# Kernel tuning notes

Hardware: AMD Instinct MI355X
Metric: run time of the kernel (lower is better)

## Reference

```python
import jax, jax.numpy as jnp
import numpy as np

CHUNK = 128


def setup_inputs() -> dict:
    key = jax.random.key(0)
    ks = jax.random.split(key, 10)
    B, L, d, n = 4, 2048, 192, 64
    sd = 1.0 / np.sqrt(d)
    return {
        "x": jax.random.normal(ks[0], (B, L, d), dtype=jnp.float32),
        "A_log": -jnp.log(2.0) + 0.1 * jax.random.normal(ks[1], (d,), dtype=jnp.float32),
        "W_B": sd * jax.random.normal(ks[2], (n, d), dtype=jnp.float32),
        "W_C": sd * jax.random.normal(ks[3], (n, d), dtype=jnp.float32),
        "W_dt": sd * jax.random.normal(ks[4], (d, d), dtype=jnp.float32),
        "b_dt": 0.1 * jax.random.normal(ks[5], (d,), dtype=jnp.float32),
        "W_xp": sd * jax.random.normal(ks[6], (2 * d, d), dtype=jnp.float32),
        "b_xp": 0.1 * jax.random.normal(ks[7], (2 * d,), dtype=jnp.float32),
        "W_out": sd * jax.random.normal(ks[8], (d, d), dtype=jnp.float32),
        "b_out": 0.1 * jax.random.normal(ks[9], (d,), dtype=jnp.float32),
    }


def reference(x, A_log, W_B, W_C, W_dt, b_dt, W_xp, b_xp, W_out, b_out):
    p = CHUNK
    b, l, d = x.shape
    n = W_B.shape[0]
    pad = (-l) % p
    xp = jnp.pad(x, ((0, 0), (0, pad), (0, 0))) if pad > 0 else x
    c = xp.shape[1] // p

    A = -jnp.exp(A_log)                                   # (d,)
    proj = xp @ W_xp.T + b_xp                             # (b, Lp, 2d)
    x_bar, z = jnp.split(proj, 2, axis=-1)
    Bm = x_bar @ W_B.T                                    # (b, Lp, n)
    Cm = x_bar @ W_C.T                                    # (b, Lp, n)
    dt = jax.nn.softplus(x_bar @ W_dt.T + b_dt)           # (b, Lp, d)
    A_bar = jnp.exp(dt * A)                               # (b, Lp, d)

    resh = lambda t: t.reshape(b, c, p, t.shape[-1])
    xc, Bc, Cc, Ac = resh(x_bar), resh(Bm), resh(Cm), resh(A_bar)

    # intra-chunk: masked decay matrix M[b,c,i,j,d]
    log_A = jnp.log(jnp.abs(Ac) + 1e-8)
    la_cum = jnp.cumsum(log_A, axis=2)                    # (b,c,p,d)
    log_M = la_cum[:, :, :, None, :] - la_cum[:, :, None, :, :]
    causal = jnp.tril(jnp.ones((p, p), dtype=x.dtype))
    M = jnp.exp(log_M) * causal[None, None, :, :, None]   # (b,c,p,p,d)
    G = jnp.einsum('bcin,bcjn->bcij', Cc, Bc)             # C_i . B_j
    # same math as einsum('bcpn,bcpnd->bcpd', C, einsum('bcijd,bcjnd->bcind', M, B x))
    y_intra = jnp.einsum('bcij,bcijd,bcjd->bcid', G, M, xc)

    # inter-chunk recurrence over chunk states
    chunk_A = jnp.prod(Ac, axis=2)                        # (b,c,d)
    chunk_states = jnp.einsum('bcpn,bcpd->bcnd', Bc, xc * Ac)

    def step(state, inp):
        ca, cs = inp                                       # (b,d), (b,n,d)
        return state * ca[:, None, :] + cs, state          # emit state BEFORE update

    _, prev = jax.lax.scan(
        step,
        jnp.zeros((b, n, d), dtype=x.dtype),
        (jnp.moveaxis(chunk_A, 1, 0), jnp.moveaxis(chunk_states, 1, 0)),
    )
    prev = jnp.moveaxis(prev, 0, 1)                       # (b,c,n,d)
    y_inter = jnp.einsum('bcpn,bcnd->bcpd', Cc, prev)

    y = (y_intra + y_inter).reshape(b, c * p, d)[:, :l]
    y = y * jax.nn.silu(z[:, :l])
    return y @ W_out.T + b_out
```

## Files before the change

kernel.cpp:

```cpp
#include <hip/hip_runtime.h>
#include <math.h>

#define TOK      8192
#define DIM      192
#define NST      64
#define PCHUNK   128
#define NCHUNKS  64
#define CPB      16
#define BATCH    4
#define SUB      32
#define NSUB     4
#define NG       4
#define NPG      16

typedef __attribute__((ext_vector_type(8))) short  bf16x8;
typedef __attribute__((ext_vector_type(4))) float  f32x4;

__device__ __forceinline__ unsigned short f2bf(float f) {
    unsigned int u = __float_as_uint(f);
    u += 0x7fff + ((u >> 16) & 1);
    return (unsigned short)(u >> 16);
}
__device__ __forceinline__ float bf2f(unsigned short h) {
    return __uint_as_float(((unsigned int)h) << 16);
}

__global__ __launch_bounds__(256)
void cast_kernel(const float* __restrict__ x,   const float* __restrict__ Wxp,
                 const float* __restrict__ WB,  const float* __restrict__ WC,
                 const float* __restrict__ Wdt, const float* __restrict__ Wout,
                 unsigned short* __restrict__ xb,     unsigned short* __restrict__ wxpb,
                 unsigned short* __restrict__ wbcdtb, unsigned short* __restrict__ woutb)
{
    int u = blockIdx.x * 256 + threadIdx.x;
    const float* src; unsigned short* dst; int idx;
    if      (u < 393216) { src = x;    dst = xb;             idx = u; }
    else if (u < 411648) { src = Wxp;  dst = wxpb;           idx = u - 393216; }
    else if (u < 414720) { src = WB;   dst = wbcdtb;         idx = u - 411648; }
    else if (u < 417792) { src = WC;   dst = wbcdtb + 12288; idx = u - 414720; }
    else if (u < 427008) { src = Wdt;  dst = wbcdtb + 24576; idx = u - 417792; }
    else if (u < 436224) { src = Wout; dst = woutb;          idx = u - 427008; }
    else return;
    float4 v = *(const float4*)(src + (size_t)idx * 4);
    ushort4 r; r.x = f2bf(v.x); r.y = f2bf(v.y); r.z = f2bf(v.z); r.w = f2bf(v.w);
    *(ushort4*)(dst + (size_t)idx * 4) = r;
}

__device__ __forceinline__
void mfma_64x64(const unsigned short* __restrict__ X, int ldx,
                const unsigned short* __restrict__ W, int K,
                int m_wave, int n0, int lr, int kg, f32x4 acc[4][4])
{
    for (int k0 = 0; k0 < K; k0 += 32) {
        bf16x8 af[4], bfr[4];
        #pragma unroll
        for (int mi = 0; mi < 4; ++mi)
            af[mi] = *(const bf16x8*)(X + (size_t)(m_wave + mi*16 + lr) * ldx + k0 + kg*8);
        #pragma unroll
        for (int ni = 0; ni < 4; ++ni)
            bfr[ni] = *(const bf16x8*)(W + (size_t)(n0 + ni*16 + lr) * K + k0 + kg*8);
        #pragma unroll
        for (int mi = 0; mi < 4; ++mi)
            #pragma unroll
            for (int ni = 0; ni < 4; ++ni)
                acc[mi][ni] = __builtin_amdgcn_mfma_f32_16x16x32_bf16(
                                  af[mi], bfr[ni], acc[mi][ni], 0, 0, 0);
    }
}

__global__ __launch_bounds__(256)
void proj_gemm(const unsigned short* __restrict__ xb,
               const unsigned short* __restrict__ wxpb,
               const float* __restrict__ b_xp,
               float* __restrict__ proj, unsigned short* __restrict__ projb)
{
    const int lane = threadIdx.x & 63, wave = threadIdx.x >> 6;
    const int m_wave = blockIdx.x * 256 + wave * 64;
    const int n0 = blockIdx.y * 64;
    const int lr = lane & 15, kg = lane >> 4;
    f32x4 acc[4][4] = {};
    mfma_64x64(xb, DIM, wxpb, DIM, m_wave, n0, lr, kg, acc);
    #pragma unroll
    for (int ni = 0; ni < 4; ++ni) {
        int col = n0 + ni*16 + lr;
        float bias = b_xp[col];
        #pragma unroll
        for (int mi = 0; mi < 4; ++mi)
            #pragma unroll
            for (int r = 0; r < 4; ++r) {
                int row = m_wave + mi*16 + kg*4 + r;
                float v = acc[mi][ni][r] + bias;
                proj [(size_t)row * 384 + col] = v;
                projb[(size_t)row * 384 + col] = f2bf(v);
            }
    }
}

__global__ __launch_bounds__(256)
void bcdt_gemm(const unsigned short* __restrict__ projb,
               const unsigned short* __restrict__ wbcdtb,
               const float* __restrict__ b_dt, const float* __restrict__ A_log,
               float* __restrict__ BC, float* __restrict__ Abar)
{
    const int lane = threadIdx.x & 63, wave = threadIdx.x >> 6;
    const int m_wave = blockIdx.x * 256 + wave * 64;
    const int n0 = blockIdx.y * 64;
    const int lr = lane & 15, kg = lane >> 4;
    f32x4 acc[4][4] = {};
    mfma_64x64(projb, 384, wbcdtb, DIM, m_wave, n0, lr, kg, acc);
    if (n0 < 128) {
        #pragma unroll
        for (int ni = 0; ni < 4; ++ni) {
            int col = n0 + ni*16 + lr;
            #pragma unroll
            for (int mi = 0; mi < 4; ++mi)
                #pragma unroll
                for (int r = 0; r < 4; ++r) {
                    int row = m_wave + mi*16 + kg*4 + r;
                    BC[(size_t)row * 128 + col] = acc[mi][ni][r];
                }
        }
    } else {
        #pragma unroll
        for (int ni = 0; ni < 4; ++ni) {
            int c2 = n0 - 128 + ni*16 + lr;
            float bias = b_dt[c2];
            float Av = -expf(A_log[c2]);
            #pragma unroll
            for (int mi = 0; mi < 4; ++mi)
                #pragma unroll
                for (int r = 0; r < 4; ++r) {
                    int row = m_wave + mi*16 + kg*4 + r;
                    float v = acc[mi][ni][r] + bias;
                    float sp = (v > 20.f) ? v : log1pf(expf(v));
                    Abar[(size_t)row * DIM + c2] = expf(sp * Av);
                }
        }
    }
}

__global__ __launch_bounds__(256)
void out_gemm(const unsigned short* __restrict__ ygb,
              const unsigned short* __restrict__ woutb,
              const float* __restrict__ b_out, float* __restrict__ out)
{
    const int lane = threadIdx.x & 63, wave = threadIdx.x >> 6;
    const int m_wave = blockIdx.x * 256 + wave * 64;
    const int n0 = blockIdx.y * 64;
    const int lr = lane & 15, kg = lane >> 4;
    f32x4 acc[4][4] = {};
    mfma_64x64(ygb, DIM, woutb, DIM, m_wave, n0, lr, kg, acc);
    #pragma unroll
    for (int ni = 0; ni < 4; ++ni) {
        int col = n0 + ni*16 + lr;
        float bias = b_out[col];
        #pragma unroll
        for (int mi = 0; mi < 4; ++mi)
            #pragma unroll
            for (int r = 0; r < 4; ++r) {
                int row = m_wave + mi*16 + kg*4 + r;
                out[(size_t)row * DIM + col] = acc[mi][ni][r] + bias;
            }
    }
}

__global__ __launch_bounds__(192)
void state_kernel(const float* __restrict__ proj,
                  const float* __restrict__ Abar,
                  const float* __restrict__ Bm,
                  float* __restrict__ S,
                  float* __restrict__ R,
                  float* __restrict__ dprod)
{
    int bc = blockIdx.x, s = blockIdx.y, g = blockIdx.z;
    int dd = threadIdx.x;
    int t0 = bc * PCHUNK + s * SUB;
    __shared__ float Bs[SUB][NPG];
    if (threadIdx.x < SUB * NPG / 4) {
        int row = threadIdx.x >> 2, c4 = threadIdx.x & 3;
        *(float4*)&Bs[row][c4 * 4] =
            *(const float4*)(Bm + (size_t)(t0 + row) * 128 + g * NPG + c4 * 4);
    }
    __syncthreads();
    float H[NPG] = {}, Rr[NPG] = {};
    float cp = 1.f;
    float a_cur = fabsf(Abar[(size_t)t0 * DIM + dd]) + 1e-8f;
    float x_cur = proj[(size_t)t0 * 384 + dd];
    for (int i = 0; i < SUB; ++i) {
        float a_nxt = 0.f, x_nxt = 0.f;
        if (i + 1 < SUB) {
            a_nxt = fabsf(Abar[(size_t)(t0 + i + 1) * DIM + dd]) + 1e-8f;
            x_nxt = proj[(size_t)(t0 + i + 1) * 384 + dd];
        }
        cp *= a_cur;
        float4 b0 = *(const float4*)&Bs[i][0];
        float4 b1 = *(const float4*)&Bs[i][4];
        float4 b2 = *(const float4*)&Bs[i][8];
        float4 b3 = *(const float4*)&Bs[i][12];
        float bb[NPG] = {b0.x,b0.y,b0.z,b0.w, b1.x,b1.y,b1.z,b1.w,
                         b2.x,b2.y,b2.z,b2.w, b3.x,b3.y,b3.z,b3.w};
        #pragma unroll
        for (int j = 0; j < NPG; ++j) {
            float u = bb[j] * x_cur;
            H[j]  = fmaf(a_cur, H[j], u);
            Rr[j] = fmaf(u, a_cur, Rr[j]);
        }
        a_cur = a_nxt; x_cur = x_nxt;
    }
    size_t base = (((size_t)(bc * NSUB + s)) * NST + g * NPG) * DIM + dd;
    #pragma unroll
    for (int j = 0; j < NPG; ++j) {
        S[base + (size_t)j * DIM] = H[j];
        R[base + (size_t)j * DIM] = Rr[j];
    }
    if (g == 0) dprod[(size_t)(bc * NSUB + s) * DIM + dd] = cp;
}

__global__ __launch_bounds__(256)
void reduce_kernel(const float* __restrict__ dprod,
                   const float* __restrict__ R,
                   float* __restrict__ cA,
                   float* __restrict__ Rsum)
{
    int u = blockIdx.x * 256 + threadIdx.x;
    const int NR = NCHUNKS * NST * 48;
    if (u < NR) {
        int dd = (u % 48) * 4;
        int nn = (u / 48) % NST;
        int bc = u / (48 * NST);
        const size_t Q2 = (size_t)NST * DIM;
        size_t so = ((size_t)(bc * NSUB) * NST + nn) * DIM + dd;
        float4 acc = {0.f, 0.f, 0.f, 0.f};
        #pragma unroll
        for (int s = 0; s < NSUB; ++s) {
            float4 v = *(const float4*)(R + so + (size_t)s * Q2);
            acc.x += v.x; acc.y += v.y; acc.z += v.z; acc.w += v.w;
        }
        *(float4*)(Rsum + ((size_t)bc * NST + nn) * DIM + dd) = acc;
    } else if (u < NR + NCHUNKS * 48) {
        int v = u - NR;
        int dd = (v % 48) * 4;
        int bc = v / 48;
        float4 acc = {1.f, 1.f, 1.f, 1.f};
        #pragma unroll
        for (int s = 0; s < NSUB; ++s) {
            float4 dp = *(const float4*)(dprod + (size_t)(bc * NSUB + s) * DIM + dd);
            acc.x *= dp.x; acc.y *= dp.y; acc.z *= dp.z; acc.w *= dp.w;
        }
        *(float4*)(cA + (size_t)bc * DIM + dd) = acc;
    }
}

__global__ __launch_bounds__(256)
void scan_kernel(const float* __restrict__ cA,
                 const float* __restrict__ Rsum,
                 float* __restrict__ prev)
{
    int v = blockIdx.x * 256 + threadIdx.x;
    if (v >= BATCH * NST * 48) return;
    int dd = (v % 48) * 4;
    int nn = (v / 48) % NST;
    int b  = v / (48 * NST);
    int bc0 = b * CPB;
    float4 st = {0.f, 0.f, 0.f, 0.f};
    float4 a_cur = *(const float4*)(cA + (size_t)bc0 * DIM + dd);
    float4 r_cur = *(const float4*)(Rsum + ((size_t)bc0 * NST + nn) * DIM + dd);
    for (int c = 0; c < CPB; ++c) {
        int bc = bc0 + c;
        float4 a_nxt = {0,0,0,0}, r_nxt = {0,0,0,0};
        if (c + 1 < CPB) {
            a_nxt = *(const float4*)(cA + (size_t)(bc + 1) * DIM + dd);
            r_nxt = *(const float4*)(Rsum + ((size_t)(bc + 1) * NST + nn) * DIM + dd);
        }
        *(float4*)(prev + ((size_t)bc * NST + nn) * DIM + dd) = st;
        st.x = fmaf(st.x, a_cur.x, r_cur.x);
        st.y = fmaf(st.y, a_cur.y, r_cur.y);
        st.z = fmaf(st.z, a_cur.z, r_cur.z);
        st.w = fmaf(st.w, a_cur.w, r_cur.w);
        a_cur = a_nxt; r_cur = r_nxt;
    }
}

__global__ __launch_bounds__(192)
void intra_kernel(const float* __restrict__ proj,
                  const float* __restrict__ Abar,
                  const float* __restrict__ Bm,
                  const float* __restrict__ Cm,
                  const float* __restrict__ prev,
                  const float* __restrict__ S,
                  const float* __restrict__ dprod,
                  unsigned short* __restrict__ p_y)
{
    int bc = blockIdx.x, s = blockIdx.y, g = blockIdx.z;
    int dd = threadIdx.x;
    int t0 = bc * PCHUNK + s * SUB;
    __shared__ float Bs[SUB][NPG];
    __shared__ float Cs[SUB][NPG];
    if (threadIdx.x < SUB * NPG / 2) {
    }
    {
        int nunits = SUB * NPG / 4;
        for (int idx = threadIdx.x; idx < 2 * nunits; idx += 192) {
            int m = idx >= nunits;
            int q = idx - m * nunits;
            int row = q >> 2, c4 = q & 3;
            const float* src = (m ? Cm : Bm) + (size_t)(t0 + row) * 128
                             + (m ? 64 : 0) + g * NPG + c4 * 4;
            float4 v = *(const float4*)src;
            if (m) *(float4*)&Cs[row][c4 * 4] = v;
            else   *(float4*)&Bs[row][c4 * 4] = v;
        }
    }
    float H[NPG] = {}, P[NPG];
    for (int k = 0; k < s; ++k) {
        float dpk = dprod[(size_t)(bc * NSUB + k) * DIM + dd];
        size_t sb = (((size_t)(bc * NSUB + k)) * NST + g * NPG) * DIM + dd;
        #pragma unroll
        for (int j = 0; j < NPG; ++j)
            H[j] = fmaf(H[j], dpk, S[sb + (size_t)j * DIM]);
    }
    #pragma unroll
    for (int j = 0; j < NPG; ++j)
        P[j] = prev[((size_t)bc * NST + g * NPG + j) * DIM + dd];
    __syncthreads();

    float a_cur = fabsf(Abar[(size_t)t0 * DIM + dd]) + 1e-8f;
    float x_cur = proj[(size_t)t0 * 384 + dd];
    for (int i = 0; i < SUB; ++i) {
        int t = t0 + i;
        float a_nxt = 0.f, x_nxt = 0.f;
        if (i + 1 < SUB) {
            a_nxt = fabsf(Abar[(size_t)(t + 1) * DIM + dd]) + 1e-8f;
            x_nxt = proj[(size_t)(t + 1) * 384 + dd];
        }
        float4 b0 = *(const float4*)&Bs[i][0];
        float4 b1 = *(const float4*)&Bs[i][4];
        float4 b2 = *(const float4*)&Bs[i][8];
        float4 b3 = *(const float4*)&Bs[i][12];
        float4 c0 = *(const float4*)&Cs[i][0];
        float4 c1 = *(const float4*)&Cs[i][4];
        float4 c2 = *(const float4*)&Cs[i][8];
        float4 c3 = *(const float4*)&Cs[i][12];
        float bb[NPG] = {b0.x,b0.y,b0.z,b0.w, b1.x,b1.y,b1.z,b1.w,
                         b2.x,b2.y,b2.z,b2.w, b3.x,b3.y,b3.z,b3.w};
        float cc[NPG] = {c0.x,c0.y,c0.z,c0.w, c1.x,c1.y,c1.z,c1.w,
                         c2.x,c2.y,c2.z,c2.w, c3.x,c3.y,c3.z,c3.w};
        float ya[4] = {0.f, 0.f, 0.f, 0.f};
        #pragma unroll
        for (int j = 0; j < NPG; ++j) {
            H[j] = fmaf(a_cur, H[j], bb[j] * x_cur);
            ya[j & 3] = fmaf(cc[j], H[j] + P[j], ya[j & 3]);
        }
        p_y[((size_t)g * TOK + t) * DIM + dd] = f2bf((ya[0] + ya[1]) + (ya[2] + ya[3]));
        a_cur = a_nxt; x_cur = x_nxt;
    }
}

__global__ __launch_bounds__(256)
void gate_kernel(const unsigned short* __restrict__ p_y,
                 const float* __restrict__ proj,
                 unsigned short* __restrict__ ygb)
{
    int v = blockIdx.x * 256 + threadIdx.x;
    if (v >= TOK * 48) return;
    int t = v / 48;
    int dd = (v % 48) * 4;
    const size_t Q = (size_t)TOK * DIM;
    size_t off = (size_t)t * DIM + dd;
    float acc[4] = {0.f, 0.f, 0.f, 0.f};
    #pragma unroll
    for (int gidx = 0; gidx < NG; ++gidx) {
        ushort4 y = *(const ushort4*)(p_y + off + (size_t)gidx * Q);
        acc[0] += bf2f(y.x); acc[1] += bf2f(y.y);
        acc[2] += bf2f(y.z); acc[3] += bf2f(y.w);
    }
    float4 z = *(const float4*)(proj + (size_t)t * 384 + DIM + dd);
    ushort4 r;
    r.x = f2bf(acc[0] * (z.x / (1.f + expf(-z.x))));
    r.y = f2bf(acc[1] * (z.y / (1.f + expf(-z.y))));
    r.z = f2bf(acc[2] * (z.z / (1.f + expf(-z.z))));
    r.w = f2bf(acc[3] * (z.w / (1.f + expf(-z.w))));
    *(ushort4*)(ygb + off) = r;
}

extern "C" void kernel_launch(void* const* d_in, const int* in_sizes, int n_in,
                              void* d_out, int out_size, void* d_ws, size_t ws_size,
                              hipStream_t stream)
{
    (void)in_sizes; (void)n_in; (void)out_size; (void)ws_size;
    const float* x     = (const float*)d_in[0];
    const float* A_log = (const float*)d_in[1];
    const float* W_B   = (const float*)d_in[2];
    const float* W_C   = (const float*)d_in[3];
    const float* W_dt  = (const float*)d_in[4];
    const float* b_dt  = (const float*)d_in[5];
    const float* W_xp  = (const float*)d_in[6];
    const float* b_xp  = (const float*)d_in[7];
    const float* W_out = (const float*)d_in[8];
    const float* b_out = (const float*)d_in[9];
    float* out = (float*)d_out;

    char* w = (char*)d_ws;
    auto take = [&](size_t bytes) { char* p = w; w += (bytes + 255) & ~(size_t)255; return p; };
    float*          proj   = (float*)         take((size_t)TOK*384*4);
    unsigned short* projb  = (unsigned short*)take((size_t)TOK*384*2);
    unsigned short* xb     = (unsigned short*)take((size_t)TOK*DIM*2);
    unsigned short* wxpb   = (unsigned short*)take((size_t)384*DIM*2);
    unsigned short* wbcdtb = (unsigned short*)take((size_t)320*DIM*2);
    unsigned short* woutb  = (unsigned short*)take((size_t)DIM*DIM*2);
    float*          BC     = (float*)         take((size_t)TOK*128*4);
    float*          Abar   = (float*)         take((size_t)TOK*DIM*4);
    float*          dprod  = (float*)         take((size_t)NCHUNKS*NSUB*DIM*4);
    float*          cAc    = (float*)         take((size_t)NCHUNKS*DIM*4);
    float*          prev   = (float*)         take((size_t)NCHUNKS*NST*DIM*4);
    float*          Rsum   = (float*)         take((size_t)NCHUNKS*NST*DIM*4);
    float*          Sarr   = (float*)         take((size_t)NCHUNKS*NSUB*NST*DIM*4);
    float*          Rarr   = (float*)         take((size_t)NCHUNKS*NSUB*NST*DIM*4);
    unsigned short* p_y    = (unsigned short*)take((size_t)NG*TOK*DIM*2);
    unsigned short* ygb    = (unsigned short*)take((size_t)TOK*DIM*2);
    const float* Bm = BC;
    const float* Cm = BC;
    dim3 blk(256);

    cast_kernel<<<dim3((436224 + 255)/256), blk, 0, stream>>>(
        x, W_xp, W_B, W_C, W_dt, W_out, xb, wxpb, wbcdtb, woutb);
    proj_gemm<<<dim3(TOK/256, 384/64), blk, 0, stream>>>(xb, wxpb, b_xp, proj, projb);
    bcdt_gemm<<<dim3(TOK/256, 320/64), blk, 0, stream>>>(projb, wbcdtb, b_dt, A_log, BC, Abar);
    state_kernel<<<dim3(NCHUNKS, NSUB, NG), dim3(192), 0, stream>>>(
        proj, Abar, Bm, Sarr, Rarr, dprod);
    reduce_kernel<<<dim3((NCHUNKS*NST*48 + NCHUNKS*48 + 255)/256), blk, 0, stream>>>(
        dprod, Rarr, cAc, Rsum);
    scan_kernel<<<dim3((BATCH*NST*48 + 255)/256), blk, 0, stream>>>(cAc, Rsum, prev);
    intra_kernel<<<dim3(NCHUNKS, NSUB, NG), dim3(192), 0, stream>>>(
        proj, Abar, Bm, Cm, prev, Sarr, dprod, p_y);
    gate_kernel<<<dim3((TOK*48 + 255)/256), blk, 0, stream>>>(p_y, proj, ygb);
    out_gemm<<<dim3(TOK/256, DIM/64), blk, 0, stream>>>(ygb, woutb, b_out, out);
}
```

Baseline: 179.2 us.

## Fold x_bar projection into B/C/dt weights and halve state groups

Precomputes combined weights W_{B,C,dt}·W_xp[:d] and the matching biases in the prep kernel, so the B/C/dt GEMM reads bf16 x directly instead of waiting on a bf16 copy of proj. The x/z GEMM now writes separate fp32 x_bar and z arrays and drops the bf16 proj output. State groups change from 4×16 to 2×32 states per thread, which halves the partial-y traffic in the gate kernel but raises register pressure in the scan kernels. The fabs on Abar is removed because exp always yields positive values. Bf16 rounding of the combined weights slightly changes numerics.

```diff
diff --git a/kernel.cpp b/kernel.cpp
--- a/kernel.cpp
+++ b/kernel.cpp
@@ -10,8 +10,8 @@
 #define BATCH    4
 #define SUB      32
 #define NSUB     4
-#define NG       4
-#define NPG      16
+#define NG       2
+#define NPG      32
 
 typedef __attribute__((ext_vector_type(8))) short  bf16x8;
 typedef __attribute__((ext_vector_type(4))) float  f32x4;
@@ -25,25 +25,52 @@
     return __uint_as_float(((unsigned int)h) << 16);
 }
 
-__global__ __launch_bounds__(256)
-void cast_kernel(const float* __restrict__ x,   const float* __restrict__ Wxp,
+#define XU      393216
+#define WXPU    18432
+#define WOUTU   9216
+#define CAST_U  (XU + WXPU + WOUTU)
+#define WCOMB_N 61440
+#define PREP_N  (CAST_U + WCOMB_N + 320)
+
+__global__ __launch_bounds__(256)
+void prep_kernel(const float* __restrict__ x,   const float* __restrict__ Wxp,
                  const float* __restrict__ WB,  const float* __restrict__ WC,
                  const float* __restrict__ Wdt, const float* __restrict__ Wout,
+                 const float* __restrict__ b_xp, const float* __restrict__ b_dt,
                  unsigned short* __restrict__ xb,     unsigned short* __restrict__ wxpb,
-                 unsigned short* __restrict__ wbcdtb, unsigned short* __restrict__ woutb)
+                 unsigned short* __restrict__ woutb,  unsigned short* __restrict__ wcombb,
+                 float* __restrict__ biasC)
 {
     int u = blockIdx.x * 256 + threadIdx.x;
-    const float* src; unsigned short* dst; int idx;
-    if      (u < 393216) { src = x;    dst = xb;             idx = u; }
-    else if (u < 411648) { src = Wxp;  dst = wxpb;           idx = u - 393216; }
-    else if (u < 414720) { src = WB;   dst = wbcdtb;         idx = u - 411648; }
-    else if (u < 417792) { src = WC;   dst = wbcdtb + 12288; idx = u - 414720; }
-    else if (u < 427008) { src = Wdt;  dst = wbcdtb + 24576; idx = u - 417792; }
-    else if (u < 436224) { src = Wout; dst = woutb;          idx = u - 427008; }
-    else return;
-    float4 v = *(const float4*)(src + (size_t)idx * 4);
-    ushort4 r; r.x = f2bf(v.x); r.y = f2bf(v.y); r.z = f2bf(v.z); r.w = f2bf(v.w);
-    *(ushort4*)(dst + (size_t)idx * 4) = r;
+    if (u < CAST_U) {
+        const float* src; unsigned short* dst; int idx;
+        if      (u < XU)          { src = x;    dst = xb;    idx = u; }
+        else if (u < XU + WXPU)   { src = Wxp;  dst = wxpb;  idx = u - XU; }
+        else                      { src = Wout; dst = woutb; idx = u - XU - WXPU; }
+        float4 v = *(const float4*)(src + (size_t)idx * 4);
+        ushort4 r; r.x = f2bf(v.x); r.y = f2bf(v.y); r.z = f2bf(v.z); r.w = f2bf(v.w);
+        *(ushort4*)(dst + (size_t)idx * 4) = r;
+    } else if (u < CAST_U + WCOMB_N) {
+        int idx = u - CAST_U;
+        int n = idx / DIM, k = idx % DIM;
+        const float* wr = (n < 64) ? WB + (size_t)n * DIM
+                        : (n < 128) ? WC + (size_t)(n - 64) * DIM
+                                    : Wdt + (size_t)(n - 128) * DIM;
+        float acc = 0.f;
+        for (int j = 0; j < DIM; ++j)
+            acc = fmaf(wr[j], Wxp[(size_t)j * DIM + k], acc);
+        wcombb[(size_t)n * DIM + k] = f2bf(acc);
+    } else if (u < PREP_N) {
+        int n = u - CAST_U - WCOMB_N;
+        const float* wr = (n < 64) ? WB + (size_t)n * DIM
+                        : (n < 128) ? WC + (size_t)(n - 64) * DIM
+                                    : Wdt + (size_t)(n - 128) * DIM;
+        float acc = 0.f;
+        for (int j = 0; j < DIM; ++j)
+            acc = fmaf(wr[j], b_xp[j], acc);
+        if (n >= 128) acc += b_dt[n - 128];
+        biasC[n] = acc;
+    }
 }
 
 __device__ __forceinline__
@@ -69,10 +96,10 @@
 }
 
 __global__ __launch_bounds__(256)
-void proj_gemm(const unsigned short* __restrict__ xb,
-               const unsigned short* __restrict__ wxpb,
-               const float* __restrict__ b_xp,
-               float* __restrict__ proj, unsigned short* __restrict__ projb)
+void xz_gemm(const unsigned short* __restrict__ xb,
+             const unsigned short* __restrict__ wxpb,
+             const float* __restrict__ b_xp,
+             float* __restrict__ xbar, float* __restrict__ zarr)
 {
     const int lane = threadIdx.x & 63, wave = threadIdx.x >> 6;
     const int m_wave = blockIdx.x * 256 + wave * 64;
@@ -80,6 +107,8 @@
     const int lr = lane & 15, kg = lane >> 4;
     f32x4 acc[4][4] = {};
     mfma_64x64(xb, DIM, wxpb, DIM, m_wave, n0, lr, kg, acc);
+    float* dst = (n0 < DIM) ? xbar : zarr;
+    int cofs = (n0 < DIM) ? 0 : DIM;
     #pragma unroll
     for (int ni = 0; ni < 4; ++ni) {
         int col = n0 + ni*16 + lr;
@@ -89,17 +118,15 @@
             #pragma unroll
             for (int r = 0; r < 4; ++r) {
                 int row = m_wave + mi*16 + kg*4 + r;
-                float v = acc[mi][ni][r] + bias;
-                proj [(size_t)row * 384 + col] = v;
-                projb[(size_t)row * 384 + col] = f2bf(v);
+                dst[(size_t)row * DIM + col - cofs] = acc[mi][ni][r] + bias;
             }
     }
 }
 
 __global__ __launch_bounds__(256)
-void bcdt_gemm(const unsigned short* __restrict__ projb,
-               const unsigned short* __restrict__ wbcdtb,
-               const float* __restrict__ b_dt, const float* __restrict__ A_log,
+void bcdt_gemm(const unsigned short* __restrict__ xb,
+               const unsigned short* __restrict__ wcombb,
+               const float* __restrict__ biasC, const float* __restrict__ A_log,
                float* __restrict__ BC, float* __restrict__ Abar)
 {
     const int lane = threadIdx.x & 63, wave = threadIdx.x >> 6;
@@ -107,24 +134,26 @@
     const int n0 = blockIdx.y * 64;
     const int lr = lane & 15, kg = lane >> 4;
     f32x4 acc[4][4] = {};
-    mfma_64x64(projb, 384, wbcdtb, DIM, m_wave, n0, lr, kg, acc);
+    mfma_64x64(xb, DIM, wcombb, DIM, m_wave, n0, lr, kg, acc);
     if (n0 < 128) {
         #pragma unroll
         for (int ni = 0; ni < 4; ++ni) {
             int col = n0 + ni*16 + lr;
+            float bias = biasC[col];
             #pragma unroll
             for (int mi = 0; mi < 4; ++mi)
                 #pragma unroll
                 for (int r = 0; r < 4; ++r) {
                     int row = m_wave + mi*16 + kg*4 + r;
-                    BC[(size_t)row * 128 + col] = acc[mi][ni][r];
+                    BC[(size_t)row * 128 + col] = acc[mi][ni][r] + bias;
                 }
         }
     } else {
         #pragma unroll
         for (int ni = 0; ni < 4; ++ni) {
-            int c2 = n0 - 128 + ni*16 + lr;
-            float bias = b_dt[c2];
+            int col = n0 + ni*16 + lr;
+            int c2 = col - 128;
+            float bias = biasC[col];
             float Av = -expf(A_log[c2]);
             #pragma unroll
             for (int mi = 0; mi < 4; ++mi)
@@ -165,7 +194,7 @@
 }
 
 __global__ __launch_bounds__(192)
-void state_kernel(const float* __restrict__ proj,
+void state_kernel(const float* __restrict__ xbar,
                   const float* __restrict__ Abar,
                   const float* __restrict__ Bm,
                   float* __restrict__ S,
@@ -176,34 +205,31 @@
     int dd = threadIdx.x;
     int t0 = bc * PCHUNK + s * SUB;
     __shared__ float Bs[SUB][NPG];
-    if (threadIdx.x < SUB * NPG / 4) {
-        int row = threadIdx.x >> 2, c4 = threadIdx.x & 3;
+    for (int q = threadIdx.x; q < SUB * NPG / 4; q += 192) {
+        int row = q >> 3, c4 = q & 7;
         *(float4*)&Bs[row][c4 * 4] =
             *(const float4*)(Bm + (size_t)(t0 + row) * 128 + g * NPG + c4 * 4);
     }
     __syncthreads();
     float H[NPG] = {}, Rr[NPG] = {};
     float cp = 1.f;
-    float a_cur = fabsf(Abar[(size_t)t0 * DIM + dd]) + 1e-8f;
-    float x_cur = proj[(size_t)t0 * 384 + dd];
+    float a_cur = Abar[(size_t)t0 * DIM + dd] + 1e-8f;
+    float x_cur = xbar[(size_t)t0 * DIM + dd];
     for (int i = 0; i < SUB; ++i) {
         float a_nxt = 0.f, x_nxt = 0.f;
         if (i + 1 < SUB) {
-            a_nxt = fabsf(Abar[(size_t)(t0 + i + 1) * DIM + dd]) + 1e-8f;
-            x_nxt = proj[(size_t)(t0 + i + 1) * 384 + dd];
+            a_nxt = Abar[(size_t)(t0 + i + 1) * DIM + dd] + 1e-8f;
+            x_nxt = xbar[(size_t)(t0 + i + 1) * DIM + dd];
         }
         cp *= a_cur;
-        float4 b0 = *(const float4*)&Bs[i][0];
-        float4 b1 = *(const float4*)&Bs[i][4];
-        float4 b2 = *(const float4*)&Bs[i][8];
-        float4 b3 = *(const float4*)&Bs[i][12];
-        float bb[NPG] = {b0.x,b0.y,b0.z,b0.w, b1.x,b1.y,b1.z,b1.w,
-                         b2.x,b2.y,b2.z,b2.w, b3.x,b3.y,b3.z,b3.w};
-        #pragma unroll
-        for (int j = 0; j < NPG; ++j) {
-            float u = bb[j] * x_cur;
-            H[j]  = fmaf(a_cur, H[j], u);
-            Rr[j] = fmaf(u, a_cur, Rr[j]);
+        #pragma unroll
+        for (int q = 0; q < NPG / 4; ++q) {
+            float4 b = *(const float4*)&Bs[i][q * 4];
+            float u0 = b.x * x_cur, u1 = b.y * x_cur, u2 = b.z * x_cur, u3 = b.w * x_cur;
+            H[q*4+0] = fmaf(a_cur, H[q*4+0], u0); Rr[q*4+0] = fmaf(u0, a_cur, Rr[q*4+0]);
+            H[q*4+1] = fmaf(a_cur, H[q*4+1], u1); Rr[q*4+1] = fmaf(u1, a_cur, Rr[q*4+1]);
+            H[q*4+2] = fmaf(a_cur, H[q*4+2], u2); Rr[q*4+2] = fmaf(u2, a_cur, Rr[q*4+2]);
+            H[q*4+3] = fmaf(a_cur, H[q*4+3], u3); Rr[q*4+3] = fmaf(u3, a_cur, Rr[q*4+3]);
         }
         a_cur = a_nxt; x_cur = x_nxt;
     }
@@ -282,10 +308,9 @@
 }
 
 __global__ __launch_bounds__(192)
-void intra_kernel(const float* __restrict__ proj,
+void intra_kernel(const float* __restrict__ xbar,
                   const float* __restrict__ Abar,
-                  const float* __restrict__ Bm,
-                  const float* __restrict__ Cm,
+                  const float* __restrict__ BC,
                   const float* __restrict__ prev,
                   const float* __restrict__ S,
                   const float* __restrict__ dprod,
@@ -296,15 +321,13 @@
     int t0 = bc * PCHUNK + s * SUB;
     __shared__ float Bs[SUB][NPG];
     __shared__ float Cs[SUB][NPG];
-    if (threadIdx.x < SUB * NPG / 2) {
-    }
     {
         int nunits = SUB * NPG / 4;
         for (int idx = threadIdx.x; idx < 2 * nunits; idx += 192) {
             int m = idx >= nunits;
             int q = idx - m * nunits;
-            int row = q >> 2, c4 = q & 3;
-            const float* src = (m ? Cm : Bm) + (size_t)(t0 + row) * 128
+            int row = q >> 3, c4 = q & 7;
+            const float* src = BC + (size_t)(t0 + row) * 128
                              + (m ? 64 : 0) + g * NPG + c4 * 4;
             float4 v = *(const float4*)src;
             if (m) *(float4*)&Cs[row][c4 * 4] = v;
@@ -324,32 +347,28 @@
         P[j] = prev[((size_t)bc * NST + g * NPG + j) * DIM + dd];
     __syncthreads();
 
-    float a_cur = fabsf(Abar[(size_t)t0 * DIM + dd]) + 1e-8f;
-    float x_cur = proj[(size_t)t0 * 384 + dd];
+    float a_cur = Abar[(size_t)t0 * DIM + dd] + 1e-8f;
+    float x_cur = xbar[(size_t)t0 * DIM + dd];
     for (int i = 0; i < SUB; ++i) {
         int t = t0 + i;
         float a_nxt = 0.f, x_nxt = 0.f;
         if (i + 1 < SUB) {
-            a_nxt = fabsf(Abar[(size_t)(t + 1) * DIM + dd]) + 1e-8f;
-            x_nxt = proj[(size_t)(t + 1) * 384 + dd];
-        }
-        float4 b0 = *(const float4*)&Bs[i][0];
-        float4 b1 = *(const float4*)&Bs[i][4];
-        float4 b2 = *(const float4*)&Bs[i][8];
-        float4 b3 = *(const float4*)&Bs[i][12];
-        float4 c0 = *(const float4*)&Cs[i][0];
-        float4 c1 = *(const float4*)&Cs[i][4];
-        float4 c2 = *(const float4*)&Cs[i][8];
-        float4 c3 = *(const float4*)&Cs[i][12];
-        float bb[NPG] = {b0.x,b0.y,b0.z,b0.w, b1.x,b1.y,b1.z,b1.w,
-                         b2.x,b2.y,b2.z,b2.w, b3.x,b3.y,b3.z,b3.w};
-        float cc[NPG] = {c0.x,c0.y,c0.z,c0.w, c1.x,c1.y,c1.z,c1.w,
-                         c2.x,c2.y,c2.z,c2.w, c3.x,c3.y,c3.z,c3.w};
+            a_nxt = Abar[(size_t)(t + 1) * DIM + dd] + 1e-8f;
+            x_nxt = xbar[(size_t)(t + 1) * DIM + dd];
+        }
         float ya[4] = {0.f, 0.f, 0.f, 0.f};
         #pragma unroll
-        for (int j = 0; j < NPG; ++j) {
-            H[j] = fmaf(a_cur, H[j], bb[j] * x_cur);
-            ya[j & 3] = fmaf(cc[j], H[j] + P[j], ya[j & 3]);
+        for (int q = 0; q < NPG / 4; ++q) {
+            float4 b = *(const float4*)&Bs[i][q * 4];
+            float4 c = *(const float4*)&Cs[i][q * 4];
+            H[q*4+0] = fmaf(a_cur, H[q*4+0], b.x * x_cur);
+            ya[0] = fmaf(c.x, H[q*4+0] + P[q*4+0], ya[0]);
+            H[q*4+1] = fmaf(a_cur, H[q*4+1], b.y * x_cur);
+            ya[1] = fmaf(c.y, H[q*4+1] + P[q*4+1], ya[1]);
+            H[q*4+2] = fmaf(a_cur, H[q*4+2], b.z * x_cur);
+            ya[2] = fmaf(c.z, H[q*4+2] + P[q*4+2], ya[2]);
+            H[q*4+3] = fmaf(a_cur, H[q*4+3], b.w * x_cur);
+            ya[3] = fmaf(c.w, H[q*4+3] + P[q*4+3], ya[3]);
         }
         p_y[((size_t)g * TOK + t) * DIM + dd] = f2bf((ya[0] + ya[1]) + (ya[2] + ya[3]));
         a_cur = a_nxt; x_cur = x_nxt;
@@ -358,7 +377,7 @@
 
 __global__ __launch_bounds__(256)
 void gate_kernel(const unsigned short* __restrict__ p_y,
-                 const float* __restrict__ proj,
+                 const float* __restrict__ zarr,
                  unsigned short* __restrict__ ygb)
 {
     int v = blockIdx.x * 256 + threadIdx.x;
@@ -367,19 +386,14 @@
     int dd = (v % 48) * 4;
     const size_t Q = (size_t)TOK * DIM;
     size_t off = (size_t)t * DIM + dd;
-    float acc[4] = {0.f, 0.f, 0.f, 0.f};
-    #pragma unroll
-    for (int gidx = 0; gidx < NG; ++gidx) {
-        ushort4 y = *(const ushort4*)(p_y + off + (size_t)gidx * Q);
-        acc[0] += bf2f(y.x); acc[1] += bf2f(y.y);
-        acc[2] += bf2f(y.z); acc[3] += bf2f(y.w);
-    }
-    float4 z = *(const float4*)(proj + (size_t)t * 384 + DIM + dd);
+    ushort4 y0 = *(const ushort4*)(p_y + off);
+    ushort4 y1 = *(const ushort4*)(p_y + off + Q);
+    float4 z = *(const float4*)(zarr + off);
     ushort4 r;
-    r.x = f2bf(acc[0] * (z.x / (1.f + expf(-z.x))));
-    r.y = f2bf(acc[1] * (z.y / (1.f + expf(-z.y))));
-    r.z = f2bf(acc[2] * (z.z / (1.f + expf(-z.z))));
-    r.w = f2bf(acc[3] * (z.w / (1.f + expf(-z.w))));
+    r.x = f2bf((bf2f(y0.x) + bf2f(y1.x)) * (z.x / (1.f + expf(-z.x))));
+    r.y = f2bf((bf2f(y0.y) + bf2f(y1.y)) * (z.y / (1.f + expf(-z.y))));
+    r.z = f2bf((bf2f(y0.z) + bf2f(y1.z)) * (z.z / (1.f + expf(-z.z))));
+    r.w = f2bf((bf2f(y0.w) + bf2f(y1.w)) * (z.w / (1.f + expf(-z.w))));
     *(ushort4*)(ygb + off) = r;
 }
 
@@ -402,12 +416,13 @@
 
     char* w = (char*)d_ws;
     auto take = [&](size_t bytes) { char* p = w; w += (bytes + 255) & ~(size_t)255; return p; };
-    float*          proj   = (float*)         take((size_t)TOK*384*4);
-    unsigned short* projb  = (unsigned short*)take((size_t)TOK*384*2);
     unsigned short* xb     = (unsigned short*)take((size_t)TOK*DIM*2);
     unsigned short* wxpb   = (unsigned short*)take((size_t)384*DIM*2);
-    unsigned short* wbcdtb = (unsigned short*)take((size_t)320*DIM*2);
     unsigned short* woutb  = (unsigned short*)take((size_t)DIM*DIM*2);
+    unsigned short* wcombb = (unsigned short*)take((size_t)320*DIM*2);
+    float*          biasC  = (float*)         take((size_t)320*4);
+    float*          xbar   = (float*)         take((size_t)TOK*DIM*4);
+    float*          zarr   = (float*)         take((size_t)TOK*DIM*4);
     float*          BC     = (float*)         take((size_t)TOK*128*4);
     float*          Abar   = (float*)         take((size_t)TOK*DIM*4);
     float*          dprod  = (float*)         take((size_t)NCHUNKS*NSUB*DIM*4);
@@ -418,21 +433,20 @@
     float*          Rarr   = (float*)         take((size_t)NCHUNKS*NSUB*NST*DIM*4);
     unsigned short* p_y    = (unsigned short*)take((size_t)NG*TOK*DIM*2);
     unsigned short* ygb    = (unsigned short*)take((size_t)TOK*DIM*2);
-    const float* Bm = BC;
-    const float* Cm = BC;
+
     dim3 blk(256);
 
-    cast_kernel<<<dim3((436224 + 255)/256), blk, 0, stream>>>(
-        x, W_xp, W_B, W_C, W_dt, W_out, xb, wxpb, wbcdtb, woutb);
-    proj_gemm<<<dim3(TOK/256, 384/64), blk, 0, stream>>>(xb, wxpb, b_xp, proj, projb);
-    bcdt_gemm<<<dim3(TOK/256, 320/64), blk, 0, stream>>>(projb, wbcdtb, b_dt, A_log, BC, Abar);
+    prep_kernel<<<dim3((PREP_N + 255)/256), blk, 0, stream>>>(
+        x, W_xp, W_B, W_C, W_dt, W_out, b_xp, b_dt, xb, wxpb, woutb, wcombb, biasC);
+    xz_gemm<<<dim3(TOK/256, 384/64), blk, 0, stream>>>(xb, wxpb, b_xp, xbar, zarr);
+    bcdt_gemm<<<dim3(TOK/256, 320/64), blk, 0, stream>>>(xb, wcombb, biasC, A_log, BC, Abar);
     state_kernel<<<dim3(NCHUNKS, NSUB, NG), dim3(192), 0, stream>>>(
-        proj, Abar, Bm, Sarr, Rarr, dprod);
+        xbar, Abar, BC, Sarr, Rarr, dprod);
     reduce_kernel<<<dim3((NCHUNKS*NST*48 + NCHUNKS*48 + 255)/256), blk, 0, stream>>>(
         dprod, Rarr, cAc, Rsum);
     scan_kernel<<<dim3((BATCH*NST*48 + 255)/256), blk, 0, stream>>>(cAc, Rsum, prev);
     intra_kernel<<<dim3(NCHUNKS, NSUB, NG), dim3(192), 0, stream>>>(
-        proj, Abar, Bm, Cm, prev, Sarr, dprod, p_y);
-    gate_kernel<<<dim3((TOK*48 + 255)/256), blk, 0, stream>>>(p_y, proj, ygb);
+        xbar, Abar, BC, prev, Sarr, dprod, p_y);
+    gate_kernel<<<dim3((TOK*48 + 255)/256), blk, 0, stream>>>(p_y, zarr, ygb);
     out_gemm<<<dim3(TOK/256, DIM/64), blk, 0, stream>>>(ygb, woutb, b_out, out);
 }
```

After: 189.1 us. 5.5% more time.
